# Optimization experiments

Hardware: AMD Instinct MI355X
Metric: run time of the kernel (lower is better)

The kernel has to match this reference:

```python
import jax, jax.numpy as jnp
import numpy as np


def setup_inputs() -> dict:
    key = jax.random.key(0)
    ks = jax.random.split(key, 5)
    B, N, F, S = 8, 128, 32, 8
    F_ = 32          # output channels
    H = 32           # kernel_network hidden width
    node_features = jax.random.normal(ks[0], (B, N, F), dtype=jnp.float32)
    fltr = jax.random.uniform(ks[1], (B, N, N), dtype=jnp.float32)
    edge_features = jax.random.normal(ks[2], (B, N, N, S), dtype=jnp.float32)
    W0 = jax.random.normal(ks[3], (S, H), dtype=jnp.float32) * (1.0 / np.sqrt(S))
    b0 = jnp.zeros((H,), dtype=jnp.float32)
    W_out = jax.random.normal(ks[4], (H, F_ * F), dtype=jnp.float32) * (1.0 / np.sqrt(H))
    b_out = jnp.zeros((F_ * F,), dtype=jnp.float32)
    bias = jnp.zeros((F_,), dtype=jnp.float32)
    return {"node_features": node_features, "fltr": fltr, "edge_features": edge_features,
            "W0": W0, "b0": b0, "W_out": W_out, "b_out": b_out, "bias": bias}


def reference(node_features, fltr, edge_features, W0, b0, W_out, b_out, bias):
    B, N, F = node_features.shape
    F_ = bias.shape[0]
    # row-normalize the filter (adjacency)
    fltr_n = fltr / jnp.maximum(jnp.sum(fltr, axis=-1, keepdims=True), 1e-11)
    # kernel-generating network over edge features: (B,N,N,S) -> (B,N,N,F_*F)
    h = jax.nn.relu(edge_features @ W0 + b0)
    kernel = (h @ W_out + b_out).reshape(B, N, N, F_, F)
    # scale by normalized filter and aggregate neighbors:
    # out[a,b,c] = sum_{i,f} fltr_n[a,b,i] * kernel[a,b,i,c,f] * nf[a,i,f]
    out = jnp.einsum('abi,abicf,aif->abc', fltr_n, kernel, node_features)
    out = out + bias  # (B,N,F_)
    return out
```

## Files before the change

### kernel.cpp

```cpp
#include <hip/hip_runtime.h>

#define Bn 8
#define Nn 128
#define Fdim 32
#define Sdim 8
#define Hdim 32
#define Fout 32

typedef float  f32x4  __attribute__((ext_vector_type(4)));
typedef short  bf16x8 __attribute__((ext_vector_type(8)));

#define PITCH 136
#define TSP   36

__device__ __forceinline__ unsigned short f2bf(float x) {
    union { float f; unsigned u; } v; v.f = x;
    return (unsigned short)((v.u + 0x7FFFu + ((v.u >> 16) & 1u)) >> 16);
}
__device__ __forceinline__ unsigned pack2(float lo, float hi) {
    return (unsigned)f2bf(lo) | ((unsigned)f2bf(hi) << 16);
}

__global__ __launch_bounds__(512, 8) void ecc_kernel(
    const float* __restrict__ nf,
    const float* __restrict__ fltr,
    const float* __restrict__ ef,
    const float* __restrict__ W0,
    const float* __restrict__ b0,
    const float* __restrict__ Wout,
    const float* __restrict__ bout,
    const float* __restrict__ bias,
    float* __restrict__ out)
{
    __shared__ __align__(16) unsigned short hT[Hdim * PITCH];
    __shared__ __align__(16) unsigned short nT[Fdim * PITCH];
    __shared__ __align__(16) float Ts[Hdim * TSP];
    __shared__ __align__(16) float qp[16 * Fdim];
    __shared__ float inv_s;

    const int t    = threadIdx.x;
    const int blk  = blockIdx.x;
    const int a    = blk >> 7;
    const int hcol = t & 31;
    const int seg  = t >> 5;

    const float* __restrict__ nfa  = nf   + (size_t)a   * (Nn * Fdim);
    const float* __restrict__ frow = fltr + (size_t)blk * Nn;
    const float* __restrict__ erow = ef   + (size_t)blk * (Nn * Sdim);

    float w0r[Sdim];
    #pragma unroll
    for (int s = 0; s < Sdim; ++s) w0r[s] = W0[s * Hdim + hcol];
    const float b0r = b0[hcol];

    if (t < 64) {
        float s = frow[t] + frow[t + 64];
        #pragma unroll
        for (int off = 32; off > 0; off >>= 1) s += __shfl_down(s, off);
        if (t == 0) inv_s = 1.0f / fmaxf(s, 1e-11f);
    }

    if (t < (Hdim * TSP) / 4) ((f32x4*)Ts)[t] = (f32x4){0.f, 0.f, 0.f, 0.f};

    {
        float x[8], q = 0.f;
        #pragma unroll
        for (int k = 0; k < 8; ++k) {
            const int i = seg * 8 + k;
            x[k] = nfa[i * Fdim + hcol];
            q += frow[i] * x[k];
        }
        unsigned* dst = (unsigned*)&nT[hcol * PITCH + seg * 8];
        #pragma unroll
        for (int k = 0; k < 8; k += 2) dst[k >> 1] = pack2(x[k], x[k + 1]);
        qp[seg * Fdim + hcol] = q;
    }

    {
        unsigned* dst = (unsigned*)&hT[hcol * PITCH + seg * 8];
        #pragma unroll 4
        for (int k = 0; k < 8; k += 2) {
            const int i0 = seg * 8 + k;
            const float4 e0a = *(const float4*)(erow + i0 * Sdim);
            const float4 e0b = *(const float4*)(erow + i0 * Sdim + 4);
            const float4 e1a = *(const float4*)(erow + i0 * Sdim + 8);
            const float4 e1b = *(const float4*)(erow + i0 * Sdim + 12);
            float a0 = b0r, a1 = b0r;
            a0 += e0a.x * w0r[0] + e0a.y * w0r[1] + e0a.z * w0r[2] + e0a.w * w0r[3];
            a0 += e0b.x * w0r[4] + e0b.y * w0r[5] + e0b.z * w0r[6] + e0b.w * w0r[7];
            a1 += e1a.x * w0r[0] + e1a.y * w0r[1] + e1a.z * w0r[2] + e1a.w * w0r[3];
            a1 += e1b.x * w0r[4] + e1b.y * w0r[5] + e1b.z * w0r[6] + e1b.w * w0r[7];
            const float h0 = fmaxf(a0, 0.0f) * frow[i0];
            const float h1 = fmaxf(a1, 0.0f) * frow[i0 + 1];
            dst[k >> 1] = pack2(h0, h1);
        }
    }
    __syncthreads();

    {
        const int w  = t >> 6, l = t & 63;
        const int lr = l & 15, lg = l >> 4;
        const int tile = w & 3, kh = w >> 2;
        const int mt = tile >> 1, nt = tile & 1;
        f32x4 acc = {0.f, 0.f, 0.f, 0.f};
        #pragma unroll
        for (int kk = 0; kk < 2; ++kk) {
            const int kt = kh * 2 + kk;
            const bf16x8 av = *(const bf16x8*)&hT[(mt * 16 + lr) * PITCH + kt * 32 + lg * 8];
            const bf16x8 bv = *(const bf16x8*)&nT[(nt * 16 + lr) * PITCH + kt * 32 + lg * 8];
            acc = __builtin_amdgcn_mfma_f32_16x16x32_bf16(av, bv, acc, 0, 0, 0);
        }
        #pragma unroll
        for (int r = 0; r < 4; ++r)
            atomicAdd(&Ts[(mt * 16 + lg * 4 + r) * TSP + nt * 16 + lr], acc[r]);
    }
    __syncthreads();

    {
        const int c = t >> 4, hp = t & 15;
        float partial = 0.f;
        #pragma unroll
        for (int hh = 0; hh < 2; ++hh) {
            const int h = hp + hh * 16;
            const float* wbase = Wout + (size_t)h * (Fout * Fdim) + c * Fdim;
            #pragma unroll 4
            for (int f4 = 0; f4 < 8; ++f4) {
                const float4 wv = *(const float4*)(wbase + f4 * 4);
                const float4 tv = *(const float4*)&Ts[h * TSP + f4 * 4];
                partial += tv.x * wv.x + tv.y * wv.y + tv.z * wv.z + tv.w * wv.w;
            }
        }
        {
            const float* bbase = bout + (size_t)c * Fdim;
            #pragma unroll 4
            for (int f4 = 0; f4 < 8; ++f4) {
                const float4 bv = *(const float4*)(bbase + f4 * 4);
                const float4 qv = *(const float4*)&qp[hp * Fdim + f4 * 4];
                partial += qv.x * bv.x + qv.y * bv.y + qv.z * bv.z + qv.w * bv.w;
            }
        }
        partial += __shfl_down(partial, 8, 16);
        partial += __shfl_down(partial, 4, 16);
        partial += __shfl_down(partial, 2, 16);
        partial += __shfl_down(partial, 1, 16);
        if (hp == 0)
            out[(size_t)blk * Fout + c] = partial * inv_s + bias[c];
    }
}

extern "C" void kernel_launch(void* const* d_in, const int* in_sizes, int n_in,
                              void* d_out, int out_size, void* d_ws, size_t ws_size,
                              hipStream_t stream) {
    const float* nf   = (const float*)d_in[0];
    const float* fltr = (const float*)d_in[1];
    const float* ef   = (const float*)d_in[2];
    const float* W0   = (const float*)d_in[3];
    const float* b0   = (const float*)d_in[4];
    const float* Wout = (const float*)d_in[5];
    const float* bout = (const float*)d_in[6];
    const float* bias = (const float*)d_in[7];
    float* out = (float*)d_out;

    ecc_kernel<<<dim3(Bn * Nn), dim3(512), 0, stream>>>(
        nf, fltr, ef, W0, b0, Wout, bout, bias, out);
}
```

Measured before the change: 99.90 us.

## Split into two kernels: per-row partial products, then MFMA GEMM with Wout

New measurement: 88.66 us. -11.3%, faster.

```diff
diff --git a/kernel.cpp b/kernel.cpp
--- a/kernel.cpp
+++ b/kernel.cpp
@@ -7,11 +7,12 @@
 #define Hdim 32
 #define Fout 32
 
+#define PITCH  72
+#define ROWLEN 1056
+#define ROW2   2112
+
 typedef float  f32x4  __attribute__((ext_vector_type(4)));
 typedef short  bf16x8 __attribute__((ext_vector_type(8)));
-
-#define PITCH 136
-#define TSP   36
 
 __device__ __forceinline__ unsigned short f2bf(float x) {
     union { float f; unsigned u; } v; v.f = x;
@@ -21,130 +22,168 @@
     return (unsigned)f2bf(lo) | ((unsigned)f2bf(hi) << 16);
 }
 
-__global__ __launch_bounds__(512, 8) void ecc_kernel(
+__global__ __launch_bounds__(256, 4) void ecc_k1(
     const float* __restrict__ nf,
     const float* __restrict__ fltr,
     const float* __restrict__ ef,
     const float* __restrict__ W0,
     const float* __restrict__ b0,
+    float* __restrict__ P)
+{
+    __shared__ __align__(16) unsigned short hT[Hdim * PITCH];
+    __shared__ __align__(16) unsigned short nT[Fdim * PITCH];
+    __shared__ float qp[8 * Fdim];
+    __shared__ float inv_s;
+
+    const int t     = threadIdx.x;
+    const int blk   = blockIdx.x;
+    const int ab    = blk >> 1, kh = blk & 1;
+    const int a     = ab >> 7;
+    const int i0    = kh * 64;
+    const int lane5 = t & 31;
+    const int seg   = t >> 5;
+
+    const float* __restrict__ nfa  = nf   + (size_t)a  * (Nn * Fdim);
+    const float* __restrict__ frow = fltr + (size_t)ab * Nn;
+    const float* __restrict__ erow = ef   + (size_t)ab * (Nn * Sdim);
+
+    float w0r[Sdim];
+    #pragma unroll
+    for (int s = 0; s < Sdim; ++s) w0r[s] = W0[s * Hdim + lane5];
+    const float b0r = b0[lane5];
+
+    if (t < 64) {
+        float s = frow[t] + frow[t + 64];
+        #pragma unroll
+        for (int off = 32; off > 0; off >>= 1) s += __shfl_down(s, off);
+        if (t == 0) inv_s = 1.0f / fmaxf(s, 1e-11f);
+    }
+
+    {
+        float x[8], q = 0.f;
+        #pragma unroll
+        for (int k = 0; k < 8; ++k) {
+            const int i = i0 + seg * 8 + k;
+            x[k] = nfa[i * Fdim + lane5];
+            q += frow[i] * x[k];
+        }
+        unsigned* dst = (unsigned*)&nT[lane5 * PITCH + seg * 8];
+        #pragma unroll
+        for (int k = 0; k < 8; k += 2) dst[k >> 1] = pack2(x[k], x[k + 1]);
+        qp[seg * Fdim + lane5] = q;
+    }
+
+    {
+        unsigned* dst = (unsigned*)&hT[lane5 * PITCH + seg * 8];
+        #pragma unroll
+        for (int k = 0; k < 8; k += 2) {
+            const int i = i0 + seg * 8 + k;
+            const float4 e0a = *(const float4*)(erow + i * Sdim);
+            const float4 e0b = *(const float4*)(erow + i * Sdim + 4);
+            const float4 e1a = *(const float4*)(erow + i * Sdim + 8);
+            const float4 e1b = *(const float4*)(erow + i * Sdim + 12);
+            float a0 = b0r, a1 = b0r;
+            a0 += e0a.x * w0r[0] + e0a.y * w0r[1] + e0a.z * w0r[2] + e0a.w * w0r[3];
+            a0 += e0b.x * w0r[4] + e0b.y * w0r[5] + e0b.z * w0r[6] + e0b.w * w0r[7];
+            a1 += e1a.x * w0r[0] + e1a.y * w0r[1] + e1a.z * w0r[2] + e1a.w * w0r[3];
+            a1 += e1b.x * w0r[4] + e1b.y * w0r[5] + e1b.z * w0r[6] + e1b.w * w0r[7];
+            const float h0 = fmaxf(a0, 0.0f) * frow[i];
+            const float h1 = fmaxf(a1, 0.0f) * frow[i + 1];
+            dst[k >> 1] = pack2(h0, h1);
+        }
+    }
+    __syncthreads();
+
+    {
+        const int w  = t >> 6, l = t & 63;
+        const int lr = l & 15, lg = l >> 4;
+        const int mt = w >> 1, nt = w & 1;
+        f32x4 acc = {0.f, 0.f, 0.f, 0.f};
+        #pragma unroll
+        for (int kt = 0; kt < 2; ++kt) {
+            const bf16x8 av = *(const bf16x8*)&hT[(mt * 16 + lr) * PITCH + kt * 32 + lg * 8];
+            const bf16x8 bv = *(const bf16x8*)&nT[(nt * 16 + lr) * PITCH + kt * 32 + lg * 8];
+            acc = __builtin_amdgcn_mfma_f32_16x16x32_bf16(av, bv, acc, 0, 0, 0);
+        }
+        const float inv = inv_s;
+        float* prow = P + (size_t)ab * ROW2 + (size_t)kh * ROWLEN;
+        #pragma unroll
+        for (int r = 0; r < 4; ++r)
+            prow[(mt * 16 + lg * 4 + r) * 32 + nt * 16 + lr] = acc[r] * inv;
+    }
+    if (t < 32) {
+        float q = 0.f;
+        #pragma unroll
+        for (int s = 0; s < 8; ++s) q += qp[s * Fdim + t];
+        P[(size_t)ab * ROW2 + (size_t)kh * ROWLEN + 1024 + t] = q * inv_s;
+    }
+}
+
+__global__ __launch_bounds__(256) void ecc_k2(
+    const float* __restrict__ P,
     const float* __restrict__ Wout,
     const float* __restrict__ bout,
     const float* __restrict__ bias,
     float* __restrict__ out)
 {
-    __shared__ __align__(16) unsigned short hT[Hdim * PITCH];
-    __shared__ __align__(16) unsigned short nT[Fdim * PITCH];
-    __shared__ __align__(16) float Ts[Hdim * TSP];
-    __shared__ __align__(16) float qp[16 * Fdim];
-    __shared__ float inv_s;
-
-    const int t    = threadIdx.x;
-    const int blk  = blockIdx.x;
-    const int a    = blk >> 7;
-    const int hcol = t & 31;
-    const int seg  = t >> 5;
-
-    const float* __restrict__ nfa  = nf   + (size_t)a   * (Nn * Fdim);
-    const float* __restrict__ frow = fltr + (size_t)blk * Nn;
-    const float* __restrict__ erow = ef   + (size_t)blk * (Nn * Sdim);
-
-    float w0r[Sdim];
+    __shared__ __align__(16) float pbuf[4 * 512];
+
+    const int t  = threadIdx.x;
+    const int w  = t >> 6, l = t & 63;
+    const int lr = l & 15, lg = l >> 4;
+    const int mtile = blockIdx.x;
+
+    const float* arow = P + (size_t)(mtile * 16 + lr) * ROW2;
+    const int ks = (w == 0) ? 0 : (8 * w + 1);
+    const int ke = 8 * w + 9;
+
+    f32x4 acc0 = {0.f, 0.f, 0.f, 0.f};
+    f32x4 acc1 = {0.f, 0.f, 0.f, 0.f};
+
+    for (int kt = ks; kt < ke; ++kt) {
+        const int k0 = kt * 32 + lg * 8;
+        const float4 a0 = *(const float4*)(arow + k0);
+        const float4 a1 = *(const float4*)(arow + k0 + 4);
+        const float4 a2 = *(const float4*)(arow + ROWLEN + k0);
+        const float4 a3 = *(const float4*)(arow + ROWLEN + k0 + 4);
+        union { bf16x8 v; unsigned u[4]; } av;
+        av.u[0] = pack2(a0.x + a2.x, a0.y + a2.y);
+        av.u[1] = pack2(a0.z + a2.z, a0.w + a2.w);
+        av.u[2] = pack2(a1.x + a3.x, a1.y + a3.y);
+        av.u[3] = pack2(a1.z + a3.z, a1.w + a3.w);
+        const float* wb = (kt < 32) ? (Wout + (size_t)kt * (Fout * Fdim)) : bout;
+        {
+            const float* p = wb + lr * Fdim + lg * 8;
+            const float4 b0v = *(const float4*)p;
+            const float4 b1v = *(const float4*)(p + 4);
+            union { bf16x8 v; unsigned u[4]; } bv;
+            bv.u[0] = pack2(b0v.x, b0v.y); bv.u[1] = pack2(b0v.z, b0v.w);
+            bv.u[2] = pack2(b1v.x, b1v.y); bv.u[3] = pack2(b1v.z, b1v.w);
+            acc0 = __builtin_amdgcn_mfma_f32_16x16x32_bf16(av.v, bv.v, acc0, 0, 0, 0);
+        }
+        {
+            const float* p = wb + (16 + lr) * Fdim + lg * 8;
+            const float4 b0v = *(const float4*)p;
+            const float4 b1v = *(const float4*)(p + 4);
+            union { bf16x8 v; unsigned u[4]; } bv;
+            bv.u[0] = pack2(b0v.x, b0v.y); bv.u[1] = pack2(b0v.z, b0v.w);
+            bv.u[2] = pack2(b1v.x, b1v.y); bv.u[3] = pack2(b1v.z, b1v.w);
+            acc1 = __builtin_amdgcn_mfma_f32_16x16x32_bf16(av.v, bv.v, acc1, 0, 0, 0);
+        }
+    }
+
     #pragma unroll
-    for (int s = 0; s < Sdim; ++s) w0r[s] = W0[s * Hdim + hcol];
-    const float b0r = b0[hcol];
-
-    if (t < 64) {
-        float s = frow[t] + frow[t + 64];
-        #pragma unroll
-        for (int off = 32; off > 0; off >>= 1) s += __shfl_down(s, off);
-        if (t == 0) inv_s = 1.0f / fmaxf(s, 1e-11f);
-    }
-
-    if (t < (Hdim * TSP) / 4) ((f32x4*)Ts)[t] = (f32x4){0.f, 0.f, 0.f, 0.f};
-
-    {
-        float x[8], q = 0.f;
-        #pragma unroll
-        for (int k = 0; k < 8; ++k) {
-            const int i = seg * 8 + k;
-            x[k] = nfa[i * Fdim + hcol];
-            q += frow[i] * x[k];
-        }
-        unsigned* dst = (unsigned*)&nT[hcol * PITCH + seg * 8];
-        #pragma unroll
-        for (int k = 0; k < 8; k += 2) dst[k >> 1] = pack2(x[k], x[k + 1]);
-        qp[seg * Fdim + hcol] = q;
-    }
-
-    {
-        unsigned* dst = (unsigned*)&hT[hcol * PITCH + seg * 8];
-        #pragma unroll 4
-        for (int k = 0; k < 8; k += 2) {
-            const int i0 = seg * 8 + k;
-            const float4 e0a = *(const float4*)(erow + i0 * Sdim);
-            const float4 e0b = *(const float4*)(erow + i0 * Sdim + 4);
-            const float4 e1a = *(const float4*)(erow + i0 * Sdim + 8);
-            const float4 e1b = *(const float4*)(erow + i0 * Sdim + 12);
-            float a0 = b0r, a1 = b0r;
-            a0 += e0a.x * w0r[0] + e0a.y * w0r[1] + e0a.z * w0r[2] + e0a.w * w0r[3];
-            a0 += e0b.x * w0r[4] + e0b.y * w0r[5] + e0b.z * w0r[6] + e0b.w * w0r[7];
-            a1 += e1a.x * w0r[0] + e1a.y * w0r[1] + e1a.z * w0r[2] + e1a.w * w0r[3];
-            a1 += e1b.x * w0r[4] + e1b.y * w0r[5] + e1b.z * w0r[6] + e1b.w * w0r[7];
-            const float h0 = fmaxf(a0, 0.0f) * frow[i0];
-            const float h1 = fmaxf(a1, 0.0f) * frow[i0 + 1];
-            dst[k >> 1] = pack2(h0, h1);
-        }
+    for (int r = 0; r < 4; ++r) {
+        pbuf[w * 512 + (lg * 4 + r) * 32 + lr]      = acc0[r];
+        pbuf[w * 512 + (lg * 4 + r) * 32 + 16 + lr] = acc1[r];
     }
     __syncthreads();
 
-    {
-        const int w  = t >> 6, l = t & 63;
-        const int lr = l & 15, lg = l >> 4;
-        const int tile = w & 3, kh = w >> 2;
-        const int mt = tile >> 1, nt = tile & 1;
-        f32x4 acc = {0.f, 0.f, 0.f, 0.f};
-        #pragma unroll
-        for (int kk = 0; kk < 2; ++kk) {
-            const int kt = kh * 2 + kk;
-            const bf16x8 av = *(const bf16x8*)&hT[(mt * 16 + lr) * PITCH + kt * 32 + lg * 8];
-            const bf16x8 bv = *(const bf16x8*)&nT[(nt * 16 + lr) * PITCH + kt * 32 + lg * 8];
-            acc = __builtin_amdgcn_mfma_f32_16x16x32_bf16(av, bv, acc, 0, 0, 0);
-        }
-        #pragma unroll
-        for (int r = 0; r < 4; ++r)
-            atomicAdd(&Ts[(mt * 16 + lg * 4 + r) * TSP + nt * 16 + lr], acc[r]);
-    }
-    __syncthreads();
-
-    {
-        const int c = t >> 4, hp = t & 15;
-        float partial = 0.f;
-        #pragma unroll
-        for (int hh = 0; hh < 2; ++hh) {
-            const int h = hp + hh * 16;
-            const float* wbase = Wout + (size_t)h * (Fout * Fdim) + c * Fdim;
-            #pragma unroll 4
-            for (int f4 = 0; f4 < 8; ++f4) {
-                const float4 wv = *(const float4*)(wbase + f4 * 4);
-                const float4 tv = *(const float4*)&Ts[h * TSP + f4 * 4];
-                partial += tv.x * wv.x + tv.y * wv.y + tv.z * wv.z + tv.w * wv.w;
-            }
-        }
-        {
-            const float* bbase = bout + (size_t)c * Fdim;
-            #pragma unroll 4
-            for (int f4 = 0; f4 < 8; ++f4) {
-                const float4 bv = *(const float4*)(bbase + f4 * 4);
-                const float4 qv = *(const float4*)&qp[hp * Fdim + f4 * 4];
-                partial += qv.x * bv.x + qv.y * bv.y + qv.z * bv.z + qv.w * bv.w;
-            }
-        }
-        partial += __shfl_down(partial, 8, 16);
-        partial += __shfl_down(partial, 4, 16);
-        partial += __shfl_down(partial, 2, 16);
-        partial += __shfl_down(partial, 1, 16);
-        if (hp == 0)
-            out[(size_t)blk * Fout + c] = partial * inv_s + bias[c];
+    #pragma unroll
+    for (int e = t; e < 512; e += 256) {
+        const int m = e >> 5, c = e & 31;
+        const float s = pbuf[e] + pbuf[512 + e] + pbuf[1024 + e] + pbuf[1536 + e] + bias[c];
+        out[(size_t)(mtile * 16 + m) * Fout + c] = s;
     }
 }
 
@@ -160,7 +199,8 @@
     const float* bout = (const float*)d_in[6];
     const float* bias = (const float*)d_in[7];
     float* out = (float*)d_out;
-
-    ecc_kernel<<<dim3(Bn * Nn), dim3(512), 0, stream>>>(
-        nf, fltr, ef, W0, b0, Wout, bout, bias, out);
-}
+    float* P   = (float*)d_ws;
+
+    ecc_k1<<<dim3(Bn * Nn * 2), dim3(256), 0, stream>>>(nf, fltr, ef, W0, b0, P);
+    ecc_k2<<<dim3(64), dim3(256), 0, stream>>>(P, Wout, bout, bias, out);
+}
```
